# Optimization experiments

Hardware: AMD Instinct MI355X
Metric: run time of the kernel (lower is better)

The kernel has to match this reference:

```python
import jax, jax.numpy as jnp
import numpy as np

N_NODES = 256
BATCH = 1024
N_LAYERS = 2  # total linear layers = N_LAYERS + 1, each followed by tanh


def setup_inputs() -> dict:
    key = jax.random.key(0)
    ks = jax.random.split(key, 4)
    scale = 1.0 / np.sqrt(N_NODES)
    x = jax.random.normal(ks[0], (BATCH, N_NODES), dtype=jnp.float32)
    # nn.Linear weights: [out_features, in_features], no bias
    W0 = jax.random.normal(ks[1], (N_NODES, N_NODES), dtype=jnp.float32) * scale
    W1 = jax.random.normal(ks[2], (N_NODES, N_NODES), dtype=jnp.float32) * scale
    W2 = jax.random.normal(ks[3], (N_NODES, N_NODES), dtype=jnp.float32) * scale
    return {"x": x, "W0": W0, "W1": W1, "W2": W2}


def reference(x, W0, W1, W2):
    # Original loop: for each node i, zero out column i of x (x @ Par with
    # Par = I - e_i e_i^T), run the 3-layer tanh MLP, keep output column i.
    # Vectorized: build all N masked copies at once.
    N = x.shape[1]
    mask = (1.0 - jnp.eye(N, dtype=x.dtype))  # [i, j]: zero col j==i
    Xm = x[None, :, :] * mask[:, None, :]     # [N, B, N]
    # nn.Linear: y = h @ W.T ; tanh after every layer (incl. last)
    h = jnp.tanh(jnp.einsum('ibn,mn->ibm', Xm, W0))
    h = jnp.tanh(jnp.einsum('ibn,mn->ibm', h, W1))
    h = jnp.tanh(jnp.einsum('ibn,mn->ibm', h, W2))  # [N, B, N]
    # f_x[b, i] = h[i, b, i]
    f_x = jnp.einsum('ibi->bi', h)
    return f_x
```

## Files before the change

### kernel.cpp

```cpp
#include <hip/hip_runtime.h>
#include <hip/hip_bf16.h>

#define N_NODES 256
#define BATCH   1024

typedef __attribute__((ext_vector_type(8))) short bf16x8;
typedef __attribute__((ext_vector_type(4))) float f32x4;

__device__ __forceinline__ float ftanh(float x) {
    float e = __builtin_amdgcn_exp2f(x * 2.8853900817779268f);
    float r = __builtin_amdgcn_rcpf(e + 1.0f);
    return fmaf(-2.0f, r, 1.0f);
}

__device__ __forceinline__ unsigned short f2bf(float f) {
    unsigned u = __float_as_uint(f);
    return (unsigned short)((u + 0x7fffu + ((u >> 16) & 1u)) >> 16);
}

__device__ __forceinline__ unsigned pack_bf2(float a, float b) {
    union { __hip_bfloat162 h; unsigned u; } cvt;
    cvt.h = __float22bfloat162_rn(make_float2(a, b));
    return cvt.u;
}

__global__ void z0_gemm(const float* __restrict__ x, const float* __restrict__ W0,
                        float* __restrict__ Z0) {
    __shared__ float xs[32][36];
    __shared__ float ws[32][36];
    int t = threadIdx.x;
    int b0 = blockIdx.x * 32, m0 = blockIdx.y * 32;
    int lr = t >> 3, lc = (t & 7) << 2;
    int tr = (t >> 4) << 1, tc = (t & 15) << 1;
    float acc00 = 0.f, acc01 = 0.f, acc10 = 0.f, acc11 = 0.f;
    for (int k0 = 0; k0 < 256; k0 += 32) {
        *(float4*)&xs[lr][lc] = *(const float4*)&x[(b0 + lr) * 256 + k0 + lc];
        *(float4*)&ws[lr][lc] = *(const float4*)&W0[(m0 + lr) * 256 + k0 + lc];
        __syncthreads();
#pragma unroll
        for (int k = 0; k < 32; ++k) {
            float a0 = xs[tr][k], a1 = xs[tr + 1][k];
            float w0v = ws[tc][k], w1v = ws[tc + 1][k];
            acc00 = fmaf(a0, w0v, acc00);
            acc01 = fmaf(a0, w1v, acc01);
            acc10 = fmaf(a1, w0v, acc10);
            acc11 = fmaf(a1, w1v, acc11);
        }
        __syncthreads();
    }
    Z0[(b0 + tr) * 256 + m0 + tc]         = acc00;
    Z0[(b0 + tr) * 256 + m0 + tc + 1]     = acc01;
    Z0[(b0 + tr + 1) * 256 + m0 + tc]     = acc10;
    Z0[(b0 + tr + 1) * 256 + m0 + tc + 1] = acc11;
}

__global__ void prep(const float* __restrict__ x, const float* __restrict__ W0,
                     const float* __restrict__ W1, float* __restrict__ xT,
                     float* __restrict__ W0col, unsigned short* __restrict__ W1bf) {
    int id = blockIdx.x * 256 + threadIdx.x;
    {
        int i = id >> 10, b = id & 1023;
        xT[id] = x[b * 256 + i];
    }
    if (id < 256 * 256) {
        int i = id >> 8, m = id & 255;
        W0col[id] = W0[m * 256 + i];
        W1bf[id] = f2bf(W1[id]);
    }
}

__launch_bounds__(256, 4)
__global__ void fused(const float* __restrict__ Z0, const float* __restrict__ xT,
                      const float* __restrict__ W0col,
                      const unsigned short* __restrict__ W1bf,
                      const float* __restrict__ W2, float* __restrict__ out) {
    __shared__ __align__(16) unsigned char h0s[64 * 512];
    __shared__ float wavepart[4][64];
    int t  = threadIdx.x;
    int r0 = blockIdx.x * 64;
    int i  = blockIdx.y;

    int wave = t >> 6, lane = t & 63;
    int lr = lane & 15, lh = lane >> 4;

    float w2v[4];
#pragma unroll
    for (int nt = 0; nt < 4; ++nt)
        w2v[nt] = W2[i * 256 + wave * 64 + nt * 16 + lr];

    {
        int rowgrp = t >> 5, chunk = t & 31;
        int col0 = chunk << 3;
        float4 w0a = *(const float4*)&W0col[i * 256 + col0];
        float4 w0b = *(const float4*)&W0col[i * 256 + col0 + 4];
        float w[8] = {w0a.x, w0a.y, w0a.z, w0a.w, w0b.x, w0b.y, w0b.z, w0b.w};
#pragma unroll
        for (int p = 0; p < 8; ++p) {
            int row = p * 8 + rowgrp;
            float xi = xT[i * 1024 + r0 + row];
            float4 za = *(const float4*)&Z0[(r0 + row) * 256 + col0];
            float4 zb = *(const float4*)&Z0[(r0 + row) * 256 + col0 + 4];
            float z[8] = {za.x, za.y, za.z, za.w, zb.x, zb.y, zb.z, zb.w};
            unsigned pk[4];
#pragma unroll
            for (int e = 0; e < 4; ++e) {
                float ha = ftanh(fmaf(-xi, w[2 * e],     z[2 * e]));
                float hb = ftanh(fmaf(-xi, w[2 * e + 1], z[2 * e + 1]));
                pk[e] = pack_bf2(ha, hb);
            }
            uint4 v = make_uint4(pk[0], pk[1], pk[2], pk[3]);
            *(uint4*)(h0s + row * 512 + (((chunk ^ (row & 31)) << 4))) = v;
        }
    }
    __syncthreads();

    f32x4 acc[4][4];
#pragma unroll
    for (int a = 0; a < 4; ++a)
#pragma unroll
        for (int b = 0; b < 4; ++b)
            acc[a][b] = (f32x4){0.f, 0.f, 0.f, 0.f};

#pragma unroll
    for (int ks = 0; ks < 8; ++ks) {
        int kk = ks * 32 + lh * 8;
        int chunk = kk >> 3;
        bf16x8 afrag[4], bfrag[4];
#pragma unroll
        for (int mt = 0; mt < 4; ++mt) {
            int row = mt * 16 + lr;
            afrag[mt] = *(const bf16x8*)(h0s + row * 512 + ((chunk ^ (row & 31)) << 4));
        }
#pragma unroll
        for (int nt = 0; nt < 4; ++nt) {
            int j = wave * 64 + nt * 16 + lr;
            bfrag[nt] = *(const bf16x8*)(W1bf + j * 256 + kk);
        }
#pragma unroll
        for (int mt = 0; mt < 4; ++mt)
#pragma unroll
            for (int nt = 0; nt < 4; ++nt)
                acc[mt][nt] = __builtin_amdgcn_mfma_f32_16x16x32_bf16(
                    afrag[mt], bfrag[nt], acc[mt][nt], 0, 0, 0);
    }

    float part[4][4];
#pragma unroll
    for (int mt = 0; mt < 4; ++mt) {
#pragma unroll
        for (int r = 0; r < 4; ++r) {
            float s = 0.f;
#pragma unroll
            for (int nt = 0; nt < 4; ++nt)
                s = fmaf(ftanh(acc[mt][nt][r]), w2v[nt], s);
            s += __shfl_xor(s, 1);
            s += __shfl_xor(s, 2);
            s += __shfl_xor(s, 4);
            s += __shfl_xor(s, 8);
            part[mt][r] = s;
        }
    }
    if (lr == 0) {
#pragma unroll
        for (int mt = 0; mt < 4; ++mt)
#pragma unroll
            for (int r = 0; r < 4; ++r)
                wavepart[wave][mt * 16 + lh * 4 + r] = part[mt][r];
    }
    __syncthreads();

    if (t < 64) {
        float s = wavepart[0][t] + wavepart[1][t] + wavepart[2][t] + wavepart[3][t];
        out[(r0 + t) * 256 + i] = ftanh(s);
    }
}

extern "C" void kernel_launch(void* const* d_in, const int* in_sizes, int n_in,
                              void* d_out, int out_size, void* d_ws, size_t ws_size,
                              hipStream_t stream) {
    const float* x  = (const float*)d_in[0];
    const float* W0 = (const float*)d_in[1];
    const float* W1 = (const float*)d_in[2];
    const float* W2 = (const float*)d_in[3];
    float* out = (float*)d_out;

    char* ws = (char*)d_ws;
    float* Z0            = (float*)ws;
    float* xT            = (float*)(ws + (1 << 20));
    float* W0col         = (float*)(ws + (2 << 20));
    unsigned short* W1bf = (unsigned short*)(ws + (2 << 20) + (256 << 10));

    z0_gemm<<<dim3(32, 8), 256, 0, stream>>>(x, W0, Z0);
    prep<<<dim3(1024), 256, 0, stream>>>(x, W0, W1, xT, W0col, W1bf);
    fused<<<dim3(16, 256), 256, 0, stream>>>(Z0, xT, W0col, W1bf, W2, out);
}
```

Measured before the change: 88.36 us.

## Merge prep into Z0 GEMM kernel and alias reduction scratch onto h0 LDS

Folds the transpose and bf16 conversion work into the Z0 GEMM kernel, so the small prep launch disappears. The fused kernel drops its separate wavepart shared array and reuses the h0 tile buffer, which needs an extra barrier. It also raises the launch-bounds occupancy hint from 4 to 5 blocks per SM. The aim is less launch overhead and more resident blocks, at the cost of possible register pressure and spills under the tighter bound.

After: 246.6 us. +179.1%, slower.

```diff
diff --git a/kernel.cpp b/kernel.cpp
--- a/kernel.cpp
+++ b/kernel.cpp
@@ -24,11 +24,27 @@
     return cvt.u;
 }
 
-__global__ void z0_gemm(const float* __restrict__ x, const float* __restrict__ W0,
-                        float* __restrict__ Z0) {
+__global__ void z0_prep(const float* __restrict__ x, const float* __restrict__ W0,
+                        const float* __restrict__ W1, float* __restrict__ Z0,
+                        float* __restrict__ xT, float* __restrict__ W0col,
+                        unsigned short* __restrict__ W1bf) {
     __shared__ float xs[32][36];
     __shared__ float ws[32][36];
     int t = threadIdx.x;
+
+    int gb = (blockIdx.y * 32 + blockIdx.x) * 256 + t;
+    {
+        int i = gb >> 8, m = gb & 255;
+        W0col[gb] = W0[m * 256 + i];
+        W1bf[gb]  = f2bf(W1[gb]);
+    }
+#pragma unroll
+    for (int r = 0; r < 4; ++r) {
+        int id = r * 65536 + gb;
+        int i = id >> 10, b = id & 1023;
+        xT[id] = x[b * 256 + i];
+    }
+
     int b0 = blockIdx.x * 32, m0 = blockIdx.y * 32;
     int lr = t >> 3, lc = (t & 7) << 2;
     int tr = (t >> 4) << 1, tc = (t & 15) << 1;
@@ -54,28 +70,13 @@
     Z0[(b0 + tr + 1) * 256 + m0 + tc + 1] = acc11;
 }
 
-__global__ void prep(const float* __restrict__ x, const float* __restrict__ W0,
-                     const float* __restrict__ W1, float* __restrict__ xT,
-                     float* __restrict__ W0col, unsigned short* __restrict__ W1bf) {
-    int id = blockIdx.x * 256 + threadIdx.x;
-    {
-        int i = id >> 10, b = id & 1023;
-        xT[id] = x[b * 256 + i];
-    }
-    if (id < 256 * 256) {
-        int i = id >> 8, m = id & 255;
-        W0col[id] = W0[m * 256 + i];
-        W1bf[id] = f2bf(W1[id]);
-    }
-}
-
-__launch_bounds__(256, 4)
+__launch_bounds__(256, 5)
 __global__ void fused(const float* __restrict__ Z0, const float* __restrict__ xT,
                       const float* __restrict__ W0col,
                       const unsigned short* __restrict__ W1bf,
                       const float* __restrict__ W2, float* __restrict__ out) {
     __shared__ __align__(16) unsigned char h0s[64 * 512];
-    __shared__ float wavepart[4][64];
+    float* wavepart = (float*)h0s;
     int t  = threadIdx.x;
     int r0 = blockIdx.x * 64;
     int i  = blockIdx.y;
@@ -160,17 +161,18 @@
             part[mt][r] = s;
         }
     }
+    __syncthreads();
     if (lr == 0) {
 #pragma unroll
         for (int mt = 0; mt < 4; ++mt)
 #pragma unroll
             for (int r = 0; r < 4; ++r)
-                wavepart[wave][mt * 16 + lh * 4 + r] = part[mt][r];
+                wavepart[wave * 64 + mt * 16 + lh * 4 + r] = part[mt][r];
     }
     __syncthreads();
 
     if (t < 64) {
-        float s = wavepart[0][t] + wavepart[1][t] + wavepart[2][t] + wavepart[3][t];
+        float s = wavepart[t] + wavepart[64 + t] + wavepart[128 + t] + wavepart[192 + t];
         out[(r0 + t) * 256 + i] = ftanh(s);
     }
 }
@@ -190,7 +192,6 @@
     float* W0col         = (float*)(ws + (2 << 20));
     unsigned short* W1bf = (unsigned short*)(ws + (2 << 20) + (256 << 10));
 
-    z0_gemm<<<dim3(32, 8), 256, 0, stream>>>(x, W0, Z0);
-    prep<<<dim3(1024), 256, 0, stream>>>(x, W0, W1, xT, W0col, W1bf);
+    z0_prep<<<dim3(32, 8), 256, 0, stream>>>(x, W0, W1, Z0, xT, W0col, W1bf);
     fused<<<dim3(16, 256), 256, 0, stream>>>(Z0, xT, W0col, W1bf, W2, out);
 }
```
